# Kernel tuning notes

Hardware: AMD Instinct MI355X
Metric: run time of the kernel (lower is better)

The kernel has to match this reference:

```python
import jax, jax.numpy as jnp
import numpy as np

DIM = 1024
HEADS = 16
DHEAD = 64
INNER = HEADS * DHEAD
EPS = 1e-5


def layer_norm(x, g, b):
    mu = jnp.mean(x, axis=-1, keepdims=True)
    var = jnp.mean(jnp.square(x - mu), axis=-1, keepdims=True)
    return (x - mu) * jax.lax.rsqrt(var + EPS) * g + b


def apply_rope(x, cos, sin):
    # x: [b, h, s, d]; cos/sin broadcast as [1, 1, s, d/2]
    d2 = x.shape[-1] // 2
    x1, x2 = x[..., :d2], x[..., d2:]
    return jnp.concatenate([x1 * cos - x2 * sin, x2 * cos + x1 * sin], axis=-1)


def setup_inputs() -> dict:
    key = jax.random.key(0)
    ks = jax.random.split(key, 10)
    B, N, S = 8, 256, 4096
    latents = jax.random.normal(ks[0], (B, N, DIM), dtype=jnp.float32)
    context = jax.random.normal(ks[1], (B, S, DIM), dtype=jnp.float32)
    cos = jax.random.uniform(ks[2], (S, DHEAD // 2), dtype=jnp.float32)
    sin = jax.random.uniform(ks[3], (S, DHEAD // 2), dtype=jnp.float32)
    init = lambda k, shp, fan_in: jax.random.normal(k, shp, dtype=jnp.float32) / np.sqrt(fan_in)
    return {
        "latents": latents,
        "context": context,
        "cos": cos,
        "sin": sin,
        "ln_lat_g": jnp.ones((DIM,), jnp.float32),
        "ln_lat_b": jnp.zeros((DIM,), jnp.float32),
        "ln_ctx_g": jnp.ones((DIM,), jnp.float32),
        "ln_ctx_b": jnp.zeros((DIM,), jnp.float32),
        "Wq": init(ks[4], (DIM, INNER), DIM),
        "Wkv": init(ks[5], (DIM, 2 * INNER), DIM),
        "Wo": init(ks[6], (INNER, DIM), INNER),
        "bo": jnp.zeros((DIM,), jnp.float32),
    }


def reference(latents, context, cos, sin, ln_lat_g, ln_lat_b, ln_ctx_g, ln_ctx_b, Wq, Wkv, Wo, bo):
    b, n, _ = latents.shape
    s = context.shape[1]
    lat = layer_norm(latents, ln_lat_g, ln_lat_b)
    ctx = layer_norm(context, ln_ctx_g, ln_ctx_b)
    q = (lat @ Wq).reshape(b, n, HEADS, DHEAD).transpose(0, 2, 1, 3)   # [b,h,n,d]
    kv = ctx @ Wkv
    k, v = jnp.split(kv, 2, axis=-1)
    k = k.reshape(b, s, HEADS, DHEAD).transpose(0, 2, 1, 3)           # [b,h,s,d]
    v = v.reshape(b, s, HEADS, DHEAD).transpose(0, 2, 1, 3)
    k = apply_rope(k, cos[None, None], sin[None, None])
    scale = DHEAD ** (-0.5)
    attn = jnp.einsum('bhnd,bhsd->bhns', q, k) * scale
    attn = jnp.clip(attn, -11.0, 11.0)
    attn = jax.nn.softmax(attn, axis=-1)
    out = jnp.einsum('bhns,bhsd->bhnd', attn, v)
    out = out.transpose(0, 2, 1, 3).reshape(b, n, INNER)
    return out @ Wo + bo
```

## Files before the change

### kernel.cpp

```cpp
#include <hip/hip_runtime.h>
#include <hip/hip_bf16.h>
#include <math.h>

#define DIM   1024
#define HEADS 16
#define DHEAD 64
#define NB    8
#define NLAT  256
#define SCTX  4096

typedef short bf16x8 __attribute__((ext_vector_type(8)));
typedef float f32x4  __attribute__((ext_vector_type(4)));

__device__ __forceinline__ unsigned short f2b(float f) {
    union { float f; unsigned u; } x; x.f = f;
    unsigned r = x.u + 0x7FFFu + ((x.u >> 16) & 1u);
    return (unsigned short)(r >> 16);
}

__device__ __forceinline__ unsigned pkbf16(float a, float b) {
    float2 f2; f2.x = a; f2.y = b;
    __hip_bfloat162 h = __float22bfloat162_rn(f2);
    union { __hip_bfloat162 h; unsigned u; } cv; cv.h = h;
    return cv.u;
}

#define LN_BLOCKS (NB * NLAT + NB * SCTX)
__global__ __launch_bounds__(256) void prep_all(
    const float* __restrict__ latents, const float* __restrict__ context,
    const float* __restrict__ g_lat, const float* __restrict__ b_lat,
    const float* __restrict__ g_ctx, const float* __restrict__ b_ctx,
    const float* __restrict__ Wq, const float* __restrict__ Wkv,
    const float* __restrict__ Wo,
    unsigned short* __restrict__ lat_b, unsigned short* __restrict__ ctx_b,
    unsigned short* __restrict__ Wqb, unsigned short* __restrict__ Wkvb,
    unsigned short* __restrict__ Wob)
{
    __shared__ unsigned short tile[32][33];
    int gb = blockIdx.x, t = threadIdx.x;
    if (gb < LN_BLOCKS) {
        const float* x; const float* g; const float* b; unsigned short* y; int r;
        if (gb < NB * NLAT) { x = latents; g = g_lat; b = b_lat; y = lat_b; r = gb; }
        else { x = context; g = g_ctx; b = b_ctx; y = ctx_b; r = gb - NB * NLAT; }
        float* ls = (float*)tile;
        float* lq = ls + 4;
        float* st = ls + 8;
        float4 v = ((const float4*)(x + (size_t)r * DIM))[t];
        float s  = v.x + v.y + v.z + v.w;
        float sq = v.x * v.x + v.y * v.y + v.z * v.z + v.w * v.w;
        #pragma unroll
        for (int off = 32; off > 0; off >>= 1) {
            s  += __shfl_down(s, off);
            sq += __shfl_down(sq, off);
        }
        int wid = t >> 6, lane = t & 63;
        if (lane == 0) { ls[wid] = s; lq[wid] = sq; }
        __syncthreads();
        if (t == 0) {
            s  = ls[0] + ls[1] + ls[2] + ls[3];
            sq = lq[0] + lq[1] + lq[2] + lq[3];
            float m   = s * (1.0f / DIM);
            float var = sq * (1.0f / DIM) - m * m;
            st[0] = m;
            st[1] = rsqrtf(var + 1e-5f);
        }
        __syncthreads();
        float mu = st[0], rs = st[1];
        float4 gg = ((const float4*)g)[t];
        float4 bb = ((const float4*)b)[t];
        ushort4 o;
        o.x = f2b((v.x - mu) * rs * gg.x + bb.x);
        o.y = f2b((v.y - mu) * rs * gg.y + bb.y);
        o.z = f2b((v.z - mu) * rs * gg.z + bb.z);
        o.w = f2b((v.w - mu) * rs * gg.w + bb.w);
        ((ushort4*)(y + (size_t)r * DIM))[t] = o;
    } else {
        int id = gb - LN_BLOCKS;
        int z = id >> 10, y = (id >> 5) & 31, xb = id & 31;
        const float* W; unsigned short* Wt; int N, coloff = 0;
        switch (z) {
            case 0: W = Wq;  Wt = Wqb;  N = DIM;     break;
            case 1: W = Wkv; Wt = Wkvb; N = 2 * DIM; break;
            case 2: W = Wkv; Wt = Wkvb; N = 2 * DIM; coloff = DIM; break;
            default: W = Wo; Wt = Wob;  N = DIM;     break;
        }
        int n0 = xb * 32 + coloff, k0 = y * 32;
        int tx = t & 31, ty = t >> 5;
        #pragma unroll
        for (int i = 0; i < 4; ++i) {
            int k = k0 + ty + i * 8;
            tile[tx][ty + i * 8] = f2b(W[(size_t)k * N + n0 + tx]);
        }
        __syncthreads();
        #pragma unroll
        for (int i = 0; i < 4; ++i) {
            int n = n0 + ty + i * 8;
            Wt[(size_t)n * DIM + k0 + tx] = tile[ty + i * 8][tx];
        }
    }
}

__global__ __launch_bounds__(256, 2) void gemm_mfma(
    const unsigned short* __restrict__ A, const unsigned short* __restrict__ Bn,
    const unsigned short* __restrict__ Aq, const unsigned short* __restrict__ Bq,
    int K, const float* __restrict__ bias,
    const float* __restrict__ cosp, const float* __restrict__ sinp,
    float* __restrict__ outf,
    unsigned short* __restrict__ outk, unsigned short* __restrict__ outv,
    unsigned short* __restrict__ outq,
    int mode, int ldc)
{
    __shared__ __align__(16) unsigned short As[128 * 64];
    __shared__ __align__(16) unsigned short Bs[128 * 64];
    int t = threadIdx.x;
    int wave = t >> 6, lane = t & 63;
    int g = blockIdx.x;
    int m_tile, n_tile;
    if (mode == 2) {
        if (g >= 4096) {
            g -= 4096; mode = 1;
            A = Aq; Bn = Bq;
            n_tile = g & 7; m_tile = g >> 3;
        } else {
            int xcd = g & 7, j = g >> 3;
            n_tile = j & 15;
            m_tile = (xcd << 5) + (j >> 4);
        }
    } else {
        n_tile = g & 7; m_tile = g >> 3;
    }
    int m_base = m_tile * 128, n_base = n_tile * 128;
    int wr = wave >> 1, wc = wave & 1;
    int quad = lane >> 4, ln = lane & 15;

    f32x4 zero = {0.f, 0.f, 0.f, 0.f};
    f32x4 acc[4][4];
    #pragma unroll
    for (int i = 0; i < 4; ++i)
        #pragma unroll
        for (int j = 0; j < 4; ++j) acc[i][j] = zero;

    const unsigned short* Ag = A  + (size_t)m_base * K;
    const unsigned short* Bg = Bn + (size_t)n_base * K;

    int srow  = lane >> 3;
    int schk  = ((lane & 7) ^ srow) * 8;

    for (int k0 = 0; k0 < K; k0 += 64) {
        __syncthreads();
        #pragma unroll
        for (int j = 0; j < 4; ++j) {
            int grp = j * 4 + wave;
            int row = grp * 8 + srow;
            __builtin_amdgcn_global_load_lds(
                (const __attribute__((address_space(1))) void*)(Ag + (size_t)row * K + k0 + schk),
                (__attribute__((address_space(3))) void*)(As + grp * 512 + lane * 8),
                16, 0, 0);
            __builtin_amdgcn_global_load_lds(
                (const __attribute__((address_space(1))) void*)(Bg + (size_t)row * K + k0 + schk),
                (__attribute__((address_space(3))) void*)(Bs + grp * 512 + lane * 8),
                16, 0, 0);
        }
        __syncthreads();
        #pragma unroll
        for (int kk = 0; kk < 2; ++kk) {
            bf16x8 af[4], bfr[4];
            int slot = ((kk * 4 + quad) ^ (ln & 7)) * 8;
            #pragma unroll
            for (int i = 0; i < 4; ++i) {
                af[i]  = *(const bf16x8*)(As + (wr * 64 + i * 16 + ln) * 64 + slot);
                bfr[i] = *(const bf16x8*)(Bs + (wc * 64 + i * 16 + ln) * 64 + slot);
            }
            #pragma unroll
            for (int i = 0; i < 4; ++i)
                #pragma unroll
                for (int j = 0; j < 4; ++j)
                    acc[i][j] = __builtin_amdgcn_mfma_f32_16x16x32_bf16(af[i], bfr[j], acc[i][j], 0, 0, 0);
        }
    }

    int cl = ln, rq = quad;
    if (mode == 2 && n_base >= DIM) {
        #pragma unroll
        for (int i = 0; i < 4; ++i) {
            int s0 = m_base + wr * 64 + i * 16 + rq * 4;
            int b  = s0 >> 12, s = s0 & 4095;
            #pragma unroll
            for (int j = 0; j < 4; ++j) {
                int n2 = n_base + wc * 64 + j * 16 + cl - DIM;
                int h = n2 >> 6, d = n2 & 63;
                ushort4 pk;
                pk.x = f2b(acc[i][j][0]); pk.y = f2b(acc[i][j][1]);
                pk.z = f2b(acc[i][j][2]); pk.w = f2b(acc[i][j][3]);
                *(ushort4*)(outv + (((size_t)(b * HEADS + h) * DHEAD + d) * SCTX) + s) = pk;
            }
        }
    } else if (mode == 2) {
        #pragma unroll
        for (int i = 0; i < 4; ++i) {
            #pragma unroll
            for (int r = 0; r < 4; ++r) {
                int m = m_base + wr * 64 + i * 16 + rq * 4 + r;
                int b = m >> 12, s = m & 4095;
                #pragma unroll
                for (int j = 0; j < 2; ++j) {
                    int n = n_base + wc * 64 + j * 16 + cl;
                    int h = n >> 6, d1 = n & 63;
                    float x1 = acc[i][j][r], x2 = acc[i][j + 2][r];
                    float c  = cosp[s * 32 + d1];
                    float sn = sinp[s * 32 + d1];
                    unsigned short* kr =
                        outk + (((size_t)(b * HEADS + h) * SCTX + s) * DHEAD) + d1;
                    kr[0]  = f2b(x1 * c - x2 * sn);
                    kr[32] = f2b(x2 * c + x1 * sn);
                }
            }
        }
    } else {
        #pragma unroll
        for (int i = 0; i < 4; ++i) {
            #pragma unroll
            for (int j = 0; j < 4; ++j) {
                #pragma unroll
                for (int r = 0; r < 4; ++r) {
                    int m = m_base + wr * 64 + i * 16 + rq * 4 + r;
                    int n = n_base + wc * 64 + j * 16 + cl;
                    float cv = acc[i][j][r];
                    if (mode == 0) {
                        outf[(size_t)m * ldc + n] = cv + bias[n];
                    } else {
                        int b = m >> 8, nn = m & 255;
                        int h = n >> 6, d = n & 63;
                        outq[(((size_t)(b * HEADS + h) * NLAT + nn) * DHEAD) + d] =
                            f2b(cv * 0.125f);
                    }
                }
            }
        }
    }
}

__global__ __launch_bounds__(256, 2) void attn_mfma(
    const unsigned short* __restrict__ qb,
    const unsigned short* __restrict__ kb,
    const unsigned short* __restrict__ vtb,
    float* __restrict__ accp,
    float* __restrict__ lp)
{
    __shared__ __align__(16) unsigned short Ks[2][64 * 64];
    __shared__ __align__(16) unsigned short Vs[2][64 * 64];
    __shared__ __align__(16) unsigned short Ps[4 * 32 * 72];

    int t = threadIdx.x, w = t >> 6, l = t & 63;
    int bh = blockIdx.x >> 3;
    int qh = (blockIdx.x >> 2) & 1;
    int sh = blockIdx.x & 3;
    int quad = l >> 4, ln = l & 15;
    int q0 = qh * 128 + w * 32;

    bf16x8 qf[2][2];
    const unsigned short* qbase = qb + ((size_t)bh * NLAT + q0) * DHEAD;
    #pragma unroll
    for (int qsub = 0; qsub < 2; ++qsub)
        #pragma unroll
        for (int kc = 0; kc < 2; ++kc)
            qf[qsub][kc] = *(const bf16x8*)(qbase + (qsub * 16 + ln) * DHEAD + kc * 32 + quad * 8);

    f32x4 acc[2][4];
    #pragma unroll
    for (int i = 0; i < 2; ++i)
        #pragma unroll
        for (int j = 0; j < 4; ++j) acc[i][j] = (f32x4){0.f, 0.f, 0.f, 0.f};
    float lacc[2] = {0.f, 0.f};

    int srow = t >> 3;
    int schk = t & 7;
    int cpos = schk ^ (srow & 7);
    const unsigned short* kgb = kb  + (size_t)bh * SCTX * DHEAD;
    const unsigned short* vgb = vtb + (size_t)bh * DHEAD * SCTX;
    unsigned short* Pw = Ps + w * 32 * 72;

    const int s_begin = sh * 1024;
    const int NT = 1024 / 64;

    uint4 kreg[2], vreg[2];
    #pragma unroll
    for (int i = 0; i < 2; ++i) {
        int row = srow + 32 * i;
        kreg[i] = *(const uint4*)(kgb + (size_t)(s_begin + row) * DHEAD + schk * 8);
        vreg[i] = *(const uint4*)(vgb + (size_t)row * SCTX + s_begin + schk * 8);
    }
    #pragma unroll
    for (int i = 0; i < 2; ++i) {
        int row = srow + 32 * i;
        *(uint4*)(&Ks[0][row * 64 + cpos * 8]) = kreg[i];
        *(uint4*)(&Vs[0][row * 64 + cpos * 8]) = vreg[i];
    }

    for (int it = 0; it < NT; ++it) {
        int buf = it & 1;
        if (it + 1 < NT) {
            int s0n = s_begin + (it + 1) * 64;
            #pragma unroll
            for (int i = 0; i < 2; ++i) {
                int row = srow + 32 * i;
                kreg[i] = *(const uint4*)(kgb + (size_t)(s0n + row) * DHEAD + schk * 8);
                vreg[i] = *(const uint4*)(vgb + (size_t)row * SCTX + s0n + schk * 8);
            }
        }
        __syncthreads();

        #pragma unroll
        for (int msub = 0; msub < 4; ++msub) {
            bf16x8 af[2];
            #pragma unroll
            for (int kc = 0; kc < 2; ++kc) {
                int sr = msub * 16 + ln;
                int ck = (4 * kc + quad) ^ (ln & 7);
                af[kc] = *(const bf16x8*)(&Ks[buf][sr * 64 + ck * 8]);
            }
            #pragma unroll
            for (int nsub = 0; nsub < 2; ++nsub) {
                f32x4 c = {0.f, 0.f, 0.f, 0.f};
                c = __builtin_amdgcn_mfma_f32_16x16x32_bf16(af[0], qf[nsub][0], c, 0, 0, 0);
                c = __builtin_amdgcn_mfma_f32_16x16x32_bf16(af[1], qf[nsub][1], c, 0, 0, 0);
                float p[4];
                #pragma unroll
                for (int r = 0; r < 4; ++r) {
                    float sc = fminf(fmaxf(c[r], -11.f), 11.f);
                    p[r] = __expf(sc - 11.f);
                    lacc[nsub] += p[r];
                }
                uint2 pk;
                pk.x = pkbf16(p[0], p[1]);
                pk.y = pkbf16(p[2], p[3]);
                *(uint2*)(Pw + (nsub * 16 + ln) * 72 + msub * 16 + quad * 4) = pk;
            }
        }
        #pragma unroll
        for (int kc = 0; kc < 2; ++kc) {
            bf16x8 pa[2];
            #pragma unroll
            for (int qsub = 0; qsub < 2; ++qsub)
                pa[qsub] = *(const bf16x8*)(Pw + (qsub * 16 + ln) * 72 + kc * 32 + quad * 8);
            #pragma unroll
            for (int dsub = 0; dsub < 4; ++dsub) {
                int dr = dsub * 16 + ln;
                int ck = (4 * kc + quad) ^ (ln & 7);
                bf16x8 vb = *(const bf16x8*)(&Vs[buf][dr * 64 + ck * 8]);
                acc[0][dsub] = __builtin_amdgcn_mfma_f32_16x16x32_bf16(pa[0], vb, acc[0][dsub], 0, 0, 0);
                acc[1][dsub] = __builtin_amdgcn_mfma_f32_16x16x32_bf16(pa[1], vb, acc[1][dsub], 0, 0, 0);
            }
        }
        if (it + 1 < NT) {
            #pragma unroll
            for (int i = 0; i < 2; ++i) {
                int row = srow + 32 * i;
                *(uint4*)(&Ks[buf ^ 1][row * 64 + cpos * 8]) = kreg[i];
                *(uint4*)(&Vs[buf ^ 1][row * 64 + cpos * 8]) = vreg[i];
            }
        }
    }

    float* accs = accp + (size_t)sh * (NB * HEADS * NLAT * DHEAD);
    float* ls   = lp   + (size_t)sh * (NB * HEADS * NLAT);

    #pragma unroll
    for (int nsub = 0; nsub < 2; ++nsub) {
        float v = lacc[nsub];
        v += __shfl_xor(v, 16);
        v += __shfl_xor(v, 32);
        if (l < 16)
            ls[bh * NLAT + q0 + nsub * 16 + l] = v;
    }
    #pragma unroll
    for (int qsub = 0; qsub < 2; ++qsub)
        #pragma unroll
        for (int dsub = 0; dsub < 4; ++dsub)
            #pragma unroll
            for (int r = 0; r < 4; ++r) {
                int qg = q0 + qsub * 16 + quad * 4 + r;
                int dg = dsub * 16 + ln;
                accs[((size_t)bh * NLAT + qg) * DHEAD + dg] = acc[qsub][dsub][r];
            }
}

__global__ __launch_bounds__(256) void attn_finalize(
    const float* __restrict__ accp, const float* __restrict__ lp,
    unsigned short* __restrict__ aob)
{
    const int ACC = NB * HEADS * NLAT * DHEAD;
    const int LSZ = NB * HEADS * NLAT;
    int idx = blockIdx.x * 256 + threadIdx.x;
    int d = idx & 63;
    int rest = idx >> 6;
    int n = rest & 255, bh = rest >> 8;
    int b = bh >> 4, h = bh & 15;
    float a = accp[idx] + accp[idx + ACC] + accp[idx + 2 * ACC] + accp[idx + 3 * ACC];
    float l = lp[rest] + lp[rest + LSZ] + lp[rest + 2 * LSZ] + lp[rest + 3 * LSZ];
    aob[(((size_t)b * NLAT + n) * HEADS + h) * DHEAD + d] = f2b(a / l);
}

extern "C" void kernel_launch(void* const* d_in, const int* in_sizes, int n_in,
                              void* d_out, int out_size, void* d_ws, size_t ws_size,
                              hipStream_t stream) {
    const float* latents  = (const float*)d_in[0];
    const float* context  = (const float*)d_in[1];
    const float* cosp     = (const float*)d_in[2];
    const float* sinp     = (const float*)d_in[3];
    const float* ln_lat_g = (const float*)d_in[4];
    const float* ln_lat_b = (const float*)d_in[5];
    const float* ln_ctx_g = (const float*)d_in[6];
    const float* ln_ctx_b = (const float*)d_in[7];
    const float* Wq  = (const float*)d_in[8];
    const float* Wkv = (const float*)d_in[9];
    const float* Wo  = (const float*)d_in[10];
    const float* bo  = (const float*)d_in[11];
    float* out = (float*)d_out;

    char* base = (char*)d_ws;
    unsigned short* lat_b = (unsigned short*)(base + 0);
    unsigned short* ctx_b = (unsigned short*)(base + 4194304);
    unsigned short* Wqb   = (unsigned short*)(base + 71303168);
    unsigned short* Wkvb  = (unsigned short*)(base + 73400320);
    unsigned short* Wob   = (unsigned short*)(base + 77594624);
    unsigned short* q_b   = (unsigned short*)(base + 79691776);
    unsigned short* k_b   = (unsigned short*)(base + 83886080);
    unsigned short* vT_b  = (unsigned short*)(base + 150994944);
    float*          accp  = (float*)(base + 218103808);
    float*          lp    = (float*)(base + 251658240);
    unsigned short* aob   = (unsigned short*)(base + 252182528);

    hipLaunchKernelGGL(prep_all, dim3(LN_BLOCKS + 4096), dim3(256), 0, stream,
                       latents, context, ln_lat_g, ln_lat_b, ln_ctx_g, ln_ctx_b,
                       Wq, Wkv, Wo, lat_b, ctx_b, Wqb, Wkvb, Wob);
    hipLaunchKernelGGL(gemm_mfma, dim3(4096 + 128), dim3(256), 0, stream,
                       ctx_b, Wkvb, lat_b, Wqb, DIM, (const float*)nullptr,
                       cosp, sinp,
                       (float*)nullptr, k_b, vT_b, q_b, 2, 0);
    hipLaunchKernelGGL(attn_mfma, dim3(NB * HEADS * 8), dim3(256), 0, stream,
                       q_b, k_b, vT_b, accp, lp);
    hipLaunchKernelGGL(attn_finalize, dim3(NB * HEADS * NLAT * DHEAD / 256), dim3(256), 0, stream,
                       accp, lp, aob);
    hipLaunchKernelGGL(gemm_mfma, dim3(128), dim3(256), 0, stream,
                       aob, Wob, (const unsigned short*)nullptr, (const unsigned short*)nullptr,
                       DIM, bo,
                       (const float*)nullptr, (const float*)nullptr,
                       out, (unsigned short*)nullptr, (unsigned short*)nullptr,
                       (unsigned short*)nullptr, 0, DIM);
}
```

Before: 522.2 us.

## Replace KV/Q projection GEMM with 256x256-tile, 8-wave pipelined MFMA kernel

Adds a new gemm256 kernel for the fused K/V and Q projections. It uses 256x256 output tiles, 512 threads, double-buffered LDS filled by direct global-to-LDS loads, and interleaves LDS reads, prefetch and MFMA quarters with setprio and barriers. The larger tiles are meant to raise arithmetic intensity and cut global traffic and load latency stalls on the dominant GEMM. The rope, V-transpose and Q epilogues are moved over, and the old gemm_mfma is reduced to the output projection only. In exchange it uses more LDS and registers per block, which lowers occupancy, and the hand-placed wait counts are fragile.

```diff
diff --git a/kernel.cpp b/kernel.cpp
--- a/kernel.cpp
+++ b/kernel.cpp
@@ -100,6 +100,208 @@
     }
 }
 
+#define GK 1024
+
+#define MFMA_Q(i0, j0)                                                         \
+    _Pragma("unroll")                                                          \
+    for (int ii = 0; ii < 4; ++ii) {                                           \
+        _Pragma("unroll")                                                      \
+        for (int jj = 0; jj < 2; ++jj) {                                       \
+            acc[(i0) + ii][(j0) + jj] = __builtin_amdgcn_mfma_f32_16x16x32_bf16( \
+                a[ii][0], b[(j0) + jj][0], acc[(i0) + ii][(j0) + jj], 0, 0, 0);  \
+            acc[(i0) + ii][(j0) + jj] = __builtin_amdgcn_mfma_f32_16x16x32_bf16( \
+                a[ii][1], b[(j0) + jj][1], acc[(i0) + ii][(j0) + jj], 0, 0, 0);  \
+        }                                                                      \
+    }
+
+__global__ __launch_bounds__(512, 2) void gemm256(
+    const unsigned short* __restrict__ Akv, const unsigned short* __restrict__ Bkv,
+    const unsigned short* __restrict__ Aq,  const unsigned short* __restrict__ Bq,
+    const float* __restrict__ cosp, const float* __restrict__ sinp,
+    unsigned short* __restrict__ outk, unsigned short* __restrict__ outv,
+    unsigned short* __restrict__ outq)
+{
+    __shared__ __align__(16) unsigned short As[2][16384];
+    __shared__ __align__(16) unsigned short Bs[2][16384];
+
+    int t = threadIdx.x;
+    int w = t >> 6, l = t & 63;
+    int wr = w >> 2, wc = w & 3;
+    int quad = l >> 4, ln = l & 15;
+
+    int g = blockIdx.x;
+    const unsigned short* A; const unsigned short* B;
+    int m_tile, n_tile, isq;
+    if (g < 1024) {
+        int xcd = g & 7, j = g >> 3;
+        n_tile = j & 7;
+        m_tile = xcd * 16 + (j >> 3);
+        A = Akv; B = Bkv; isq = 0;
+    } else {
+        g -= 1024;
+        n_tile = g & 3;
+        m_tile = g >> 2;
+        A = Aq; B = Bq; isq = 1;
+    }
+    int m_base = m_tile * 256, n_base = n_tile * 256;
+    const unsigned short* Ag = A + (size_t)m_base * GK;
+    const unsigned short* Bg = B + (size_t)n_base * GK;
+
+    f32x4 acc[8][4];
+    {
+        f32x4 zero = {0.f, 0.f, 0.f, 0.f};
+        #pragma unroll
+        for (int i = 0; i < 8; ++i)
+            #pragma unroll
+            for (int j = 0; j < 4; ++j) acc[i][j] = zero;
+    }
+
+    int srow = l >> 3;
+    int schk = ((l & 7) ^ srow) * 8;
+
+    auto STAGE = [&](const unsigned short* src, int k0, unsigned short* dst) {
+        #pragma unroll
+        for (int jj = 0; jj < 2; ++jj) {
+            int row = jj * 64 + w * 8 + srow;
+            __builtin_amdgcn_global_load_lds(
+                (const __attribute__((address_space(1))) void*)(src + (size_t)row * GK + k0 + schk),
+                (__attribute__((address_space(3))) void*)(dst + row * 64 + (l & 7) * 8),
+                16, 0, 0);
+        }
+    };
+
+    STAGE(Ag,                     0, As[0]);
+    STAGE(Ag + 128 * (size_t)GK,  0, As[0] + 8192);
+    STAGE(Bg,                     0, Bs[0]);
+    STAGE(Bg + 128 * (size_t)GK,  0, Bs[0] + 8192);
+    STAGE(Bg,                    64, Bs[1]);
+    STAGE(Bg + 128 * (size_t)GK, 64, Bs[1] + 8192);
+    asm volatile("s_waitcnt vmcnt(4)" ::: "memory");
+    __builtin_amdgcn_s_barrier();
+
+    for (int kt = 0; kt < 16; ++kt) {
+        int buf = kt & 1;
+        const unsigned short* Ab = As[buf] + wr * 8192;
+        const unsigned short* Bb = Bs[buf] + (wc >> 1) * 8192;
+        int bloc = (wc & 1) * 64;
+        int xs = ln & 7;
+        bf16x8 a[4][2], b[4][2];
+
+        #pragma unroll
+        for (int i = 0; i < 4; ++i)
+            #pragma unroll
+            for (int kk = 0; kk < 2; ++kk)
+                a[i][kk] = *(const bf16x8*)(Ab + (i * 16 + ln) * 64 + (((kk * 4 + quad) ^ xs) << 3));
+        #pragma unroll
+        for (int j = 0; j < 2; ++j)
+            #pragma unroll
+            for (int kk = 0; kk < 2; ++kk)
+                b[j][kk] = *(const bf16x8*)(Bb + (bloc + j * 16 + ln) * 64 + (((kk * 4 + quad) ^ xs) << 3));
+        if (kt + 1 < 16) {
+            int k0 = (kt + 1) * 64;
+            STAGE(Ag,                    k0, As[buf ^ 1]);
+            STAGE(Ag + 128 * (size_t)GK, k0, As[buf ^ 1] + 8192);
+        }
+        __builtin_amdgcn_s_barrier();
+        asm volatile("s_waitcnt lgkmcnt(0)" ::: "memory");
+        __builtin_amdgcn_sched_barrier(0);
+        __builtin_amdgcn_s_setprio(1);
+        MFMA_Q(0, 0)
+        __builtin_amdgcn_s_setprio(0);
+        __builtin_amdgcn_s_barrier();
+
+        #pragma unroll
+        for (int j = 0; j < 2; ++j)
+            #pragma unroll
+            for (int kk = 0; kk < 2; ++kk)
+                b[2 + j][kk] = *(const bf16x8*)(Bb + (bloc + (2 + j) * 16 + ln) * 64 + (((kk * 4 + quad) ^ xs) << 3));
+        __builtin_amdgcn_s_barrier();
+        asm volatile("s_waitcnt lgkmcnt(0)" ::: "memory");
+        __builtin_amdgcn_sched_barrier(0);
+        __builtin_amdgcn_s_setprio(1);
+        MFMA_Q(0, 2)
+        __builtin_amdgcn_s_setprio(0);
+        __builtin_amdgcn_s_barrier();
+
+        #pragma unroll
+        for (int i = 0; i < 4; ++i)
+            #pragma unroll
+            for (int kk = 0; kk < 2; ++kk)
+                a[i][kk] = *(const bf16x8*)(Ab + ((4 + i) * 16 + ln) * 64 + (((kk * 4 + quad) ^ xs) << 3));
+        if (kt + 2 < 16) STAGE(Bg, (kt + 2) * 64, Bs[buf]);
+        __builtin_amdgcn_s_barrier();
+        asm volatile("s_waitcnt lgkmcnt(0)" ::: "memory");
+        __builtin_amdgcn_sched_barrier(0);
+        __builtin_amdgcn_s_setprio(1);
+        MFMA_Q(4, 2)
+        __builtin_amdgcn_s_setprio(0);
+        __builtin_amdgcn_s_barrier();
+
+        if (kt + 2 < 16) STAGE(Bg + 128 * (size_t)GK, (kt + 2) * 64, Bs[buf] + 8192);
+        __builtin_amdgcn_s_barrier();
+        __builtin_amdgcn_s_setprio(1);
+        MFMA_Q(4, 0)
+        __builtin_amdgcn_s_setprio(0);
+        if (kt + 2 < 16) asm volatile("s_waitcnt vmcnt(4)" ::: "memory");
+        else             asm volatile("s_waitcnt vmcnt(0)" ::: "memory");
+        __builtin_amdgcn_s_barrier();
+    }
+
+    if (!isq) {
+        if (n_base >= DIM) {
+            #pragma unroll
+            for (int i = 0; i < 8; ++i) {
+                int s0 = m_base + wr * 128 + i * 16 + quad * 4;
+                int bb = s0 >> 12, s = s0 & 4095;
+                #pragma unroll
+                for (int j = 0; j < 4; ++j) {
+                    int n2 = n_base + wc * 64 + j * 16 + ln - DIM;
+                    int h = n2 >> 6, d = n2 & 63;
+                    ushort4 pk;
+                    pk.x = f2b(acc[i][j][0]); pk.y = f2b(acc[i][j][1]);
+                    pk.z = f2b(acc[i][j][2]); pk.w = f2b(acc[i][j][3]);
+                    *(ushort4*)(outv + (((size_t)(bb * HEADS + h) * DHEAD + d) * SCTX) + s) = pk;
+                }
+            }
+        } else {
+            #pragma unroll
+            for (int i = 0; i < 8; ++i) {
+                #pragma unroll
+                for (int r = 0; r < 4; ++r) {
+                    int m = m_base + wr * 128 + i * 16 + quad * 4 + r;
+                    int bb = m >> 12, s = m & 4095;
+                    #pragma unroll
+                    for (int j = 0; j < 2; ++j) {
+                        int n = n_base + wc * 64 + j * 16 + ln;
+                        int h = n >> 6, d1 = n & 63;
+                        float x1 = acc[i][j][r], x2 = acc[i][j + 2][r];
+                        float c  = cosp[s * 32 + d1];
+                        float sn = sinp[s * 32 + d1];
+                        unsigned short* kr =
+                            outk + (((size_t)(bb * HEADS + h) * SCTX + s) * DHEAD) + d1;
+                        kr[0]  = f2b(x1 * c - x2 * sn);
+                        kr[32] = f2b(x2 * c + x1 * sn);
+                    }
+                }
+            }
+        }
+    } else {
+        #pragma unroll
+        for (int i = 0; i < 8; ++i)
+            #pragma unroll
+            for (int j = 0; j < 4; ++j)
+                #pragma unroll
+                for (int r = 0; r < 4; ++r) {
+                    int m = m_base + wr * 128 + i * 16 + quad * 4 + r;
+                    int n = n_base + wc * 64 + j * 16 + ln;
+                    int bb = m >> 8, nn = m & 255;
+                    int h = n >> 6, d = n & 63;
+                    outq[(((size_t)(bb * HEADS + h) * NLAT + nn) * DHEAD) + d] =
+                        f2b(acc[i][j][r] * 0.125f);
+                }
+    }
+}
+
 __global__ __launch_bounds__(256, 2) void gemm_mfma(
     const unsigned short* __restrict__ A, const unsigned short* __restrict__ Bn,
     const unsigned short* __restrict__ Aq, const unsigned short* __restrict__ Bq,
@@ -116,19 +318,7 @@
     int wave = t >> 6, lane = t & 63;
     int g = blockIdx.x;
     int m_tile, n_tile;
-    if (mode == 2) {
-        if (g >= 4096) {
-            g -= 4096; mode = 1;
-            A = Aq; Bn = Bq;
-            n_tile = g & 7; m_tile = g >> 3;
-        } else {
-            int xcd = g & 7, j = g >> 3;
-            n_tile = j & 15;
-            m_tile = (xcd << 5) + (j >> 4);
-        }
-    } else {
-        n_tile = g & 7; m_tile = g >> 3;
-    }
+    n_tile = g & 7; m_tile = g >> 3;
     int m_base = m_tile * 128, n_base = n_tile * 128;
     int wr = wave >> 1, wc = wave & 1;
     int quad = lane >> 4, ln = lane & 15;
@@ -180,61 +370,15 @@
     }
 
     int cl = ln, rq = quad;
-    if (mode == 2 && n_base >= DIM) {
-        #pragma unroll
-        for (int i = 0; i < 4; ++i) {
-            int s0 = m_base + wr * 64 + i * 16 + rq * 4;
-            int b  = s0 >> 12, s = s0 & 4095;
-            #pragma unroll
-            for (int j = 0; j < 4; ++j) {
-                int n2 = n_base + wc * 64 + j * 16 + cl - DIM;
-                int h = n2 >> 6, d = n2 & 63;
-                ushort4 pk;
-                pk.x = f2b(acc[i][j][0]); pk.y = f2b(acc[i][j][1]);
-                pk.z = f2b(acc[i][j][2]); pk.w = f2b(acc[i][j][3]);
-                *(ushort4*)(outv + (((size_t)(b * HEADS + h) * DHEAD + d) * SCTX) + s) = pk;
-            }
-        }
-    } else if (mode == 2) {
-        #pragma unroll
-        for (int i = 0; i < 4; ++i) {
+    #pragma unroll
+    for (int i = 0; i < 4; ++i) {
+        #pragma unroll
+        for (int j = 0; j < 4; ++j) {
             #pragma unroll
             for (int r = 0; r < 4; ++r) {
                 int m = m_base + wr * 64 + i * 16 + rq * 4 + r;
-                int b = m >> 12, s = m & 4095;
-                #pragma unroll
-                for (int j = 0; j < 2; ++j) {
-                    int n = n_base + wc * 64 + j * 16 + cl;
-                    int h = n >> 6, d1 = n & 63;
-                    float x1 = acc[i][j][r], x2 = acc[i][j + 2][r];
-                    float c  = cosp[s * 32 + d1];
-                    float sn = sinp[s * 32 + d1];
-                    unsigned short* kr =
-                        outk + (((size_t)(b * HEADS + h) * SCTX + s) * DHEAD) + d1;
-                    kr[0]  = f2b(x1 * c - x2 * sn);
-                    kr[32] = f2b(x2 * c + x1 * sn);
-                }
-            }
-        }
-    } else {
-        #pragma unroll
-        for (int i = 0; i < 4; ++i) {
-            #pragma unroll
-            for (int j = 0; j < 4; ++j) {
-                #pragma unroll
-                for (int r = 0; r < 4; ++r) {
-                    int m = m_base + wr * 64 + i * 16 + rq * 4 + r;
-                    int n = n_base + wc * 64 + j * 16 + cl;
-                    float cv = acc[i][j][r];
-                    if (mode == 0) {
-                        outf[(size_t)m * ldc + n] = cv + bias[n];
-                    } else {
-                        int b = m >> 8, nn = m & 255;
-                        int h = n >> 6, d = n & 63;
-                        outq[(((size_t)(b * HEADS + h) * NLAT + nn) * DHEAD) + d] =
-                            f2b(cv * 0.125f);
-                    }
-                }
+                int n = n_base + wc * 64 + j * 16 + cl;
+                outf[(size_t)m * ldc + n] = acc[i][j][r] + bias[n];
             }
         }
     }
@@ -434,10 +578,8 @@
     hipLaunchKernelGGL(prep_all, dim3(LN_BLOCKS + 4096), dim3(256), 0, stream,
                        latents, context, ln_lat_g, ln_lat_b, ln_ctx_g, ln_ctx_b,
                        Wq, Wkv, Wo, lat_b, ctx_b, Wqb, Wkvb, Wob);
-    hipLaunchKernelGGL(gemm_mfma, dim3(4096 + 128), dim3(256), 0, stream,
-                       ctx_b, Wkvb, lat_b, Wqb, DIM, (const float*)nullptr,
-                       cosp, sinp,
-                       (float*)nullptr, k_b, vT_b, q_b, 2, 0);
+    hipLaunchKernelGGL(gemm256, dim3(1024 + 32), dim3(512), 0, stream,
+                       ctx_b, Wkvb, lat_b, Wqb, cosp, sinp, k_b, vT_b, q_b);
     hipLaunchKernelGGL(attn_mfma, dim3(NB * HEADS * 8), dim3(256), 0, stream,
                        q_b, k_b, vT_b, accp, lp);
     hipLaunchKernelGGL(attn_finalize, dim3(NB * HEADS * NLAT * DHEAD / 256), dim3(256), 0, stream,
```

After: 536.2 us. 1.03x slower.
